# Kernel optimization log

Measured on AMD Instinct MI355X. Metric: run time of the kernel, lower is better.

## Reference

```python
import jax, jax.numpy as jnp
import numpy as np

N_QUBITS = 11
DIM = 2 ** N_QUBITS
N_LAYERS = 6  # the circuit repeats the RY/CZ block 6 times


def _apply_ry(state, wire, theta):
    """Apply RY(theta) on `wire`. state: [N] + [2]*N_QUBITS (real, since RY/CZ are real).
    theta is scalar (shared weight) or [N] (per-sample input angle)."""
    half = theta * 0.5
    c, s = jnp.cos(half), jnp.sin(half)
    if c.ndim == 1:  # per-sample angle -> broadcast over remaining qubit axes
        bshape = (c.shape[0],) + (1,) * (N_QUBITS - 1)
        c = c.reshape(bshape)
        s = s.reshape(bshape)
    st = jnp.moveaxis(state, wire + 1, -1)  # [..., 2]
    s0, s1 = st[..., 0], st[..., 1]
    # RY = [[cos, -sin], [sin, cos]] acting on the qubit amplitude pair
    st = jnp.stack([c * s0 - s * s1, s * s0 + c * s1], axis=-1)
    return jnp.moveaxis(st, -1, wire + 1)


def _apply_cz(state, w1, w2):
    """CZ: flip sign of amplitudes where both qubits are |1>."""
    def bit(w):
        shp = [1] * (N_QUBITS + 1)
        shp[w + 1] = 2
        return jnp.array([0.0, 1.0], state.dtype).reshape(shp)
    sign = 1.0 - 2.0 * bit(w1) * bit(w2)
    return state * sign


def _circuit(angles, weights):
    # angles: [N, N_QUBITS] per-sample RY input angles; weights: [N_QUBITS]
    N = angles.shape[0]
    state = jnp.zeros((N, DIM), angles.dtype).at[:, 0].set(1.0)  # |0...0>
    state = state.reshape((N,) + (2,) * N_QUBITS)
    for i in range(N_QUBITS):
        state = _apply_ry(state, i, angles[:, i])
    for _ in range(N_LAYERS):
        for i in range(N_QUBITS):
            state = _apply_ry(state, i, weights[i])
            state = _apply_cz(state, i, (i + 1) % N_QUBITS)
    probs = state.reshape(N, DIM) ** 2  # real state -> |amp|^2
    # PauliZ expectation per wire; wire 0 is the most-significant bit (PennyLane order)
    bits = (jnp.arange(DIM)[:, None] >> jnp.arange(N_QUBITS - 1, -1, -1)[None, :]) & 1
    z = (1.0 - 2.0 * bits).astype(angles.dtype)  # [DIM, N_QUBITS]
    return probs @ z  # [N, N_QUBITS]


def setup_inputs() -> dict:
    key = jax.random.key(0)
    kx, kw = jax.random.split(key)
    x = jax.random.normal(kx, (8, 256, 16), dtype=jnp.float32)
    weights = jax.random.normal(kw, (N_QUBITS,), dtype=jnp.float32)
    return {"x": x, "weights": weights}


def reference(x, weights):
    B, T, _ = x.shape
    # every (b, t) sample is an independent circuit -> batch them all together
    angles = x[:, :, :N_QUBITS].reshape(B * T, N_QUBITS)
    out = _circuit(angles, weights)  # [B*T, N_QUBITS]
    return out.reshape(B, T, N_QUBITS)
```

## Files before the change

kernel.cpp:

```cpp
#include <hip/hip_runtime.h>

#define NQ 11


typedef float f32x2 __attribute__((ext_vector_type(2)));

__device__ __forceinline__ f32x2 b2(float s) { f32x2 r; r.x = s; r.y = s; return r; }
__device__ __forceinline__ f32x2 fma2(f32x2 a, f32x2 b, f32x2 c) {
    return __builtin_elementwise_fma(a, b, c);
}

template <int CTRL>
__device__ __forceinline__ float dpp_mov(float x) {
    const int xi = __builtin_bit_cast(int, x);
    return __builtin_bit_cast(float,
        __builtin_amdgcn_update_dpp(xi, xi, CTRL, 0xf, 0xf, false));
}
#define DPP_XOR1 0xB1
#define DPP_XOR2 0x4E
#define DPP_XOR3 0x1B
#define DPP_XOR7 0x141
#define DPP_XOR8 0x128

#define RY_K_F(KB, KSB, C, S)                                                \
    _Pragma("unroll")                                                        \
    for (int g = 0; g < 8; ++g) {                                            \
        const int k0 = ((g >> (KB)) << ((KB) + 1)) | (g & ((1 << (KB)) - 1));\
        const int k1 = k0 | (1 << (KB));                                     \
        const f32x2 a_ = v2[k0], b_ = v2[k1];                                \
        const f32x2 Cv = b2(C), Sv = b2(S);                                  \
        if (k0 & (KSB)) {                                   \
            v2[k0] = fma2(Cv, a_, Sv * b_);                                  \
            v2[k1] = fma2(Sv, a_, -(Cv * b_));                               \
        } else {                                                             \
            v2[k0] = fma2(Cv, a_, -(Sv * b_));                               \
            v2[k1] = fma2(Sv, a_, Cv * b_);                                  \
        }                                                                    \
    }

#define RY_LANE2(PGETX, CV, SV)                                              \
    _Pragma("unroll")                                                        \
    for (int k = 0; k < 16; ++k) {                                           \
        f32x2 pa_;                                                           \
        pa_.x = PGETX(v2[k].x);                                              \
        pa_.y = PGETX(v2[k].y);                                              \
        v2[k] = fma2(CV, v2[k], (SV) * pa_);                                 \
    }

__global__ __launch_bounds__(256, 2) void qru_kernel(
    const float* __restrict__ x,
    const float* __restrict__ w,
    float* __restrict__ out)
{
    const int lane = threadIdx.x & 63;
    const int n    = blockIdx.x * 4 + (threadIdx.x >> 6);

    const float4 xa = *(const float4*)(x + n * 16);
    const float4 xb = *(const float4*)(x + n * 16 + 4);
    const float4 xc = *(const float4*)(x + n * 16 + 8);
    const float xv[NQ] = {xa.x, xa.y, xa.z, xa.w, xb.x, xb.y, xb.z, xb.w,
                          xc.x, xc.y, xc.z};
    float ci[NQ], si[NQ];
#pragma unroll
    for (int q = 0; q < NQ; ++q) {
        const float h = xv[q] * 0.5f;
        si[q] = __sinf(h); ci[q] = __cosf(h);
    }
    float cw[NQ], sw[NQ];
#pragma unroll
    for (int q = 0; q < NQ; ++q) {
        const float h = w[q] * 0.5f;
        sw[q] = __sinf(h); cw[q] = __cosf(h);
    }

    const float laneF =
        ((lane & 32) ? si[5]  : ci[5])  *
        ((lane & 16) ? si[6]  : ci[6])  *
        ((lane & 8)  ? si[7]  : ci[7])  *
        ((lane & 4)  ? si[8]  : ci[8])  *
        ((lane & 2)  ? si[9]  : ci[9])  *
        ((lane & 1)  ? si[10] : ci[10]);

    f32x2 v2[16];
#pragma unroll
    for (int k = 0; k < 16; ++k) {
        const float base = laneF * ((k & 8) ? si[0] : ci[0])
                                 * ((k & 4) ? si[1] : ci[1])
                                 * ((k & 2) ? si[2] : ci[2])
                                 * ((k & 1) ? si[3] : ci[3]);
        v2[k].x = base * ci[4];
        v2[k].y = base * si[4];
    }

    const float X0m = (lane & 1) ?  sw[0] : -sw[0];
    const float Y0m = (lane & 1) ? -cw[0] :  cw[0];
    const float SS5 = (lane & 32) ?  sw[5] : -sw[5];
    const float C5m = (lane & 32) ? -cw[5] :  cw[5];
    f32x2 Cv5; Cv5.x = cw[5]; Cv5.y = C5m;
    f32x2 Sv5; Sv5.x = SS5;   Sv5.y = sw[5];
    const f32x2 C6v  = b2(((lane & 48) == 48) ? -cw[6]  : cw[6]);
    const f32x2 S6v  = b2((lane & 48) ? sw[6]  : -sw[6]);
    const f32x2 C7v  = b2(((lane & 24) == 24) ? -cw[7]  : cw[7]);
    const f32x2 S7v  = b2((lane & 24) ? sw[7]  : -sw[7]);
    const f32x2 C8v  = b2(((lane & 12) == 12) ? -cw[8]  : cw[8]);
    const f32x2 S8v  = b2((lane & 12) ? sw[8]  : -sw[8]);
    const f32x2 C9v  = b2(((lane & 6)  == 6)  ? -cw[9]  : cw[9]);
    const f32x2 S9v  = b2((lane & 6)  ? sw[9]  : -sw[9]);
    const f32x2 C10v = b2(((lane & 3)  == 3)  ? -cw[10] : cw[10]);
    const f32x2 S10v = b2((lane & 3)  ? sw[10] : -sw[10]);

    f32x2 C4p; C4p.x = cw[4]; C4p.y =  cw[4];
    f32x2 S4p; S4p.x = -sw[4]; S4p.y = sw[4];
    f32x2 C4m; C4m.x = cw[4]; C4m.y = -cw[4];
    f32x2 S4m; S4m.x = sw[4]; S4m.y =  sw[4];

    auto shfl32 = [](float t) { return __shfl_xor(t, 32); };
    auto shfl16 = [](float t) { return __shfl_xor(t, 16); };
    auto dppx8  = [](float t) { return dpp_mov<DPP_XOR8>(t); };
    auto dppx4  = [](float t) { return dpp_mov<DPP_XOR3>(dpp_mov<DPP_XOR7>(t)); };
    auto dppx2  = [](float t) { return dpp_mov<DPP_XOR2>(t); };
    auto dppx1  = [](float t) { return dpp_mov<DPP_XOR1>(t); };

    auto layer = [&](float X0, float Y0) {
        {
            const f32x2 c0 = b2(cw[0]), s0 = b2(sw[0]);
            const f32x2 x0 = b2(X0),    y0 = b2(Y0);
#pragma unroll
            for (int k = 0; k < 8; ++k) {
                const f32x2 a_ = v2[k], b_ = v2[k | 8];
                v2[k]     = fma2(c0, a_, x0 * b_);
                v2[k | 8] = fma2(s0, a_, y0 * b_);
            }
        }
        RY_K_F(2, 8, cw[1], sw[1])
        RY_K_F(1, 4, cw[2], sw[2])
        RY_K_F(0, 2, cw[3], sw[3])

#pragma unroll
        for (int k = 0; k < 16; ++k) {
            const f32x2 s_ = __builtin_shufflevector(v2[k], v2[k], 1, 0);
            v2[k] = (k & 1) ? fma2(C4m, v2[k], S4m * s_)
                            : fma2(C4p, v2[k], S4p * s_);
        }

        RY_LANE2(shfl32, Cv5, Sv5)
        RY_LANE2(shfl16, C6v, S6v)
        RY_LANE2(dppx8,  C7v, S7v)
        RY_LANE2(dppx4,  C8v, S8v)
        RY_LANE2(dppx2,  C9v, S9v)
        RY_LANE2(dppx1,  C10v, S10v)
    };

    layer(-sw[0], cw[0]);
#pragma unroll 1
    for (int l = 1; l < 6; ++l) layer(X0m, Y0m);

    f32x2 T = b2(0.f), A3 = b2(0.f), A2 = b2(0.f), A1 = b2(0.f), A0 = b2(0.f);
#pragma unroll
    for (int k = 0; k < 16; ++k) {
        const f32x2 p = v2[k] * v2[k];
        T = T + p;
        if (k & 8) A3 = A3 + p;
        if (k & 4) A2 = A2 + p;
        if (k & 2) A1 = A1 + p;
        if (k & 1) A0 = A0 + p;
    }
    const float tot = T.x + T.y;

    float q[NQ];
    q[0] = tot - 2.f * (A3.x + A3.y);
    q[1] = tot - 2.f * (A2.x + A2.y);
    q[2] = tot - 2.f * (A1.x + A1.y);
    q[3] = tot - 2.f * (A0.x + A0.y);
    q[4] = tot - 2.f * T.y;
    q[5]  = (lane & 32) ? -tot : tot;
    q[6]  = (lane & 16) ? -tot : tot;
    q[7]  = (lane & 8)  ? -tot : tot;
    q[8]  = (lane & 4)  ? -tot : tot;
    q[9]  = (lane & 2)  ? -tot : tot;
    q[10] = (lane & 1)  ? -tot : tot;

#pragma unroll
    for (int wq = 0; wq < NQ; ++wq) {
        float a = q[wq];
        a += __shfl_xor(a, 32);
        a += __shfl_xor(a, 16);
        a += dpp_mov<DPP_XOR8>(a);
        a += dpp_mov<DPP_XOR3>(dpp_mov<DPP_XOR7>(a));
        a += dpp_mov<DPP_XOR2>(a);
        a += dpp_mov<DPP_XOR1>(a);
        q[wq] = a;
    }

    if (lane == 0) {
#pragma unroll
        for (int wq = 0; wq < NQ; ++wq) out[n * 11 + wq] = q[wq];
    }
}

extern "C" void kernel_launch(void* const* d_in, const int* in_sizes, int n_in,
                              void* d_out, int out_size, void* d_ws, size_t ws_size,
                              hipStream_t stream) {
    const float* x = (const float*)d_in[0];
    const float* w = (const float*)d_in[1];
    float* out = (float*)d_out;

    qru_kernel<<<512, 256, 0, stream>>>(x, w, out);
}
```

Before: 25.65 us.

## Process two circuits per wavefront to increase ILP and halve grid size

```diff
diff --git a/kernel.cpp b/kernel.cpp
--- a/kernel.cpp
+++ b/kernel.cpp
@@ -22,49 +22,79 @@
 #define DPP_XOR7 0x141
 #define DPP_XOR8 0x128
 
-#define RY_K_F(KB, KSB, C, S)                                                \
-    _Pragma("unroll")                                                        \
-    for (int g = 0; g < 8; ++g) {                                            \
-        const int k0 = ((g >> (KB)) << ((KB) + 1)) | (g & ((1 << (KB)) - 1));\
-        const int k1 = k0 | (1 << (KB));                                     \
-        const f32x2 a_ = v2[k0], b_ = v2[k1];                                \
+#define RY_K_F2(KB, KSB, C, S)                                               \
+    {                                                                        \
         const f32x2 Cv = b2(C), Sv = b2(S);                                  \
-        if (k0 & (KSB)) {                                   \
-            v2[k0] = fma2(Cv, a_, Sv * b_);                                  \
-            v2[k1] = fma2(Sv, a_, -(Cv * b_));                               \
-        } else {                                                             \
-            v2[k0] = fma2(Cv, a_, -(Sv * b_));                               \
-            v2[k1] = fma2(Sv, a_, Cv * b_);                                  \
+        _Pragma("unroll")                                                    \
+        for (int g = 0; g < 8; ++g) {                                        \
+            const int k0 = ((g >> (KB)) << ((KB) + 1)) | (g & ((1 << (KB)) - 1)); \
+            const int k1 = k0 | (1 << (KB));                                 \
+            const f32x2 aA = vA[k0], bA = vA[k1];                            \
+            const f32x2 aB = vB[k0], bB = vB[k1];                            \
+            if (k0 & (KSB)) {                                                \
+                vA[k0] = fma2(Cv, aA, Sv * bA);                              \
+                vA[k1] = fma2(Sv, aA, -(Cv * bA));                           \
+                vB[k0] = fma2(Cv, aB, Sv * bB);                              \
+                vB[k1] = fma2(Sv, aB, -(Cv * bB));                           \
+            } else {                                                         \
+                vA[k0] = fma2(Cv, aA, -(Sv * bA));                           \
+                vA[k1] = fma2(Sv, aA, Cv * bA);                              \
+                vB[k0] = fma2(Cv, aB, -(Sv * bB));                           \
+                vB[k1] = fma2(Sv, aB, Cv * bB);                              \
+            }                                                                \
         }                                                                    \
     }
 
-#define RY_LANE2(PGETX, CV, SV)                                              \
+#define RY_DS2(SHFL, CV, SV)                                                 \
+    {                                                                        \
+        f32x2 pA[16], pB[16];                                                \
+        _Pragma("unroll")                                                    \
+        for (int k = 0; k < 16; ++k) {                                       \
+            pA[k].x = SHFL(vA[k].x); pA[k].y = SHFL(vA[k].y);                \
+            pB[k].x = SHFL(vB[k].x); pB[k].y = SHFL(vB[k].y);                \
+        }                                                                    \
+        _Pragma("unroll")                                                    \
+        for (int k = 0; k < 16; ++k) {                                       \
+            vA[k] = fma2(CV, vA[k], (SV) * pA[k]);                           \
+            vB[k] = fma2(CV, vB[k], (SV) * pB[k]);                           \
+        }                                                                    \
+    }
+
+#define RY_DPP2(PGETX, CV, SV)                                               \
     _Pragma("unroll")                                                        \
     for (int k = 0; k < 16; ++k) {                                           \
-        f32x2 pa_;                                                           \
-        pa_.x = PGETX(v2[k].x);                                              \
-        pa_.y = PGETX(v2[k].y);                                              \
-        v2[k] = fma2(CV, v2[k], (SV) * pa_);                                 \
-    }
-
-__global__ __launch_bounds__(256, 2) void qru_kernel(
+        f32x2 pa, pb;                                                        \
+        pa.x = PGETX(vA[k].x); pa.y = PGETX(vA[k].y);                        \
+        pb.x = PGETX(vB[k].x); pb.y = PGETX(vB[k].y);                        \
+        vA[k] = fma2(CV, vA[k], (SV) * pa);                                  \
+        vB[k] = fma2(CV, vB[k], (SV) * pb);                                  \
+    }
+
+__global__ __launch_bounds__(256, 1) void qru_kernel(
     const float* __restrict__ x,
     const float* __restrict__ w,
     float* __restrict__ out)
 {
     const int lane = threadIdx.x & 63;
-    const int n    = blockIdx.x * 4 + (threadIdx.x >> 6);
-
-    const float4 xa = *(const float4*)(x + n * 16);
-    const float4 xb = *(const float4*)(x + n * 16 + 4);
-    const float4 xc = *(const float4*)(x + n * 16 + 8);
-    const float xv[NQ] = {xa.x, xa.y, xa.z, xa.w, xb.x, xb.y, xb.z, xb.w,
-                          xc.x, xc.y, xc.z};
-    float ci[NQ], si[NQ];
+    const int g    = blockIdx.x * 4 + (threadIdx.x >> 6);
+    const int nA   = 2 * g, nB = 2 * g + 1;
+
+    const float4 a0 = *(const float4*)(x + nA * 16);
+    const float4 a1 = *(const float4*)(x + nA * 16 + 4);
+    const float4 a2 = *(const float4*)(x + nA * 16 + 8);
+    const float4 b0 = *(const float4*)(x + nB * 16);
+    const float4 b1 = *(const float4*)(x + nB * 16 + 4);
+    const float4 b2_ = *(const float4*)(x + nB * 16 + 8);
+    const float xvA[NQ] = {a0.x, a0.y, a0.z, a0.w, a1.x, a1.y, a1.z, a1.w,
+                           a2.x, a2.y, a2.z};
+    const float xvB[NQ] = {b0.x, b0.y, b0.z, b0.w, b1.x, b1.y, b1.z, b1.w,
+                           b2_.x, b2_.y, b2_.z};
+    float ciA[NQ], siA[NQ], ciB[NQ], siB[NQ];
 #pragma unroll
     for (int q = 0; q < NQ; ++q) {
-        const float h = xv[q] * 0.5f;
-        si[q] = __sinf(h); ci[q] = __cosf(h);
+        const float hA = xvA[q] * 0.5f, hB = xvB[q] * 0.5f;
+        siA[q] = __sinf(hA); ciA[q] = __cosf(hA);
+        siB[q] = __sinf(hB); ciB[q] = __cosf(hB);
     }
     float cw[NQ], sw[NQ];
 #pragma unroll
@@ -73,23 +103,36 @@
         sw[q] = __sinf(h); cw[q] = __cosf(h);
     }
 
-    const float laneF =
-        ((lane & 32) ? si[5]  : ci[5])  *
-        ((lane & 16) ? si[6]  : ci[6])  *
-        ((lane & 8)  ? si[7]  : ci[7])  *
-        ((lane & 4)  ? si[8]  : ci[8])  *
-        ((lane & 2)  ? si[9]  : ci[9])  *
-        ((lane & 1)  ? si[10] : ci[10]);
-
-    f32x2 v2[16];
+    const float laneFA =
+        ((lane & 32) ? siA[5]  : ciA[5])  *
+        ((lane & 16) ? siA[6]  : ciA[6])  *
+        ((lane & 8)  ? siA[7]  : ciA[7])  *
+        ((lane & 4)  ? siA[8]  : ciA[8])  *
+        ((lane & 2)  ? siA[9]  : ciA[9])  *
+        ((lane & 1)  ? siA[10] : ciA[10]);
+    const float laneFB =
+        ((lane & 32) ? siB[5]  : ciB[5])  *
+        ((lane & 16) ? siB[6]  : ciB[6])  *
+        ((lane & 8)  ? siB[7]  : ciB[7])  *
+        ((lane & 4)  ? siB[8]  : ciB[8])  *
+        ((lane & 2)  ? siB[9]  : ciB[9])  *
+        ((lane & 1)  ? siB[10] : ciB[10]);
+
+    f32x2 vA[16], vB[16];
 #pragma unroll
     for (int k = 0; k < 16; ++k) {
-        const float base = laneF * ((k & 8) ? si[0] : ci[0])
-                                 * ((k & 4) ? si[1] : ci[1])
-                                 * ((k & 2) ? si[2] : ci[2])
-                                 * ((k & 1) ? si[3] : ci[3]);
-        v2[k].x = base * ci[4];
-        v2[k].y = base * si[4];
+        const float bA = laneFA * ((k & 8) ? siA[0] : ciA[0])
+                                * ((k & 4) ? siA[1] : ciA[1])
+                                * ((k & 2) ? siA[2] : ciA[2])
+                                * ((k & 1) ? siA[3] : ciA[3]);
+        vA[k].x = bA * ciA[4];
+        vA[k].y = bA * siA[4];
+        const float bB = laneFB * ((k & 8) ? siB[0] : ciB[0])
+                                * ((k & 4) ? siB[1] : ciB[1])
+                                * ((k & 2) ? siB[2] : ciB[2])
+                                * ((k & 1) ? siB[3] : ciB[3]);
+        vB[k].x = bB * ciB[4];
+        vB[k].y = bB * siB[4];
     }
 
     const float X0m = (lane & 1) ?  sw[0] : -sw[0];
@@ -109,10 +152,10 @@
     const f32x2 C10v = b2(((lane & 3)  == 3)  ? -cw[10] : cw[10]);
     const f32x2 S10v = b2((lane & 3)  ? sw[10] : -sw[10]);
 
-    f32x2 C4p; C4p.x = cw[4]; C4p.y =  cw[4];
-    f32x2 S4p; S4p.x = -sw[4]; S4p.y = sw[4];
-    f32x2 C4m; C4m.x = cw[4]; C4m.y = -cw[4];
-    f32x2 S4m; S4m.x = sw[4]; S4m.y =  sw[4];
+    f32x2 C4p; C4p.x = cw[4];  C4p.y =  cw[4];
+    f32x2 S4p; S4p.x = -sw[4]; S4p.y =  sw[4];
+    f32x2 C4m; C4m.x = cw[4];  C4m.y = -cw[4];
+    f32x2 S4m; S4m.x = sw[4];  S4m.y =  sw[4];
 
     auto shfl32 = [](float t) { return __shfl_xor(t, 32); };
     auto shfl16 = [](float t) { return __shfl_xor(t, 16); };
@@ -127,74 +170,94 @@
             const f32x2 x0 = b2(X0),    y0 = b2(Y0);
 #pragma unroll
             for (int k = 0; k < 8; ++k) {
-                const f32x2 a_ = v2[k], b_ = v2[k | 8];
-                v2[k]     = fma2(c0, a_, x0 * b_);
-                v2[k | 8] = fma2(s0, a_, y0 * b_);
+                const f32x2 aA = vA[k], bA = vA[k | 8];
+                vA[k]     = fma2(c0, aA, x0 * bA);
+                vA[k | 8] = fma2(s0, aA, y0 * bA);
+                const f32x2 aB = vB[k], bB = vB[k | 8];
+                vB[k]     = fma2(c0, aB, x0 * bB);
+                vB[k | 8] = fma2(s0, aB, y0 * bB);
             }
         }
-        RY_K_F(2, 8, cw[1], sw[1])
-        RY_K_F(1, 4, cw[2], sw[2])
-        RY_K_F(0, 2, cw[3], sw[3])
+        RY_K_F2(2, 8, cw[1], sw[1])
+        RY_K_F2(1, 4, cw[2], sw[2])
+        RY_K_F2(0, 2, cw[3], sw[3])
 
 #pragma unroll
         for (int k = 0; k < 16; ++k) {
-            const f32x2 s_ = __builtin_shufflevector(v2[k], v2[k], 1, 0);
-            v2[k] = (k & 1) ? fma2(C4m, v2[k], S4m * s_)
-                            : fma2(C4p, v2[k], S4p * s_);
+            const f32x2 sA = __builtin_shufflevector(vA[k], vA[k], 1, 0);
+            const f32x2 sB = __builtin_shufflevector(vB[k], vB[k], 1, 0);
+            vA[k] = (k & 1) ? fma2(C4m, vA[k], S4m * sA)
+                            : fma2(C4p, vA[k], S4p * sA);
+            vB[k] = (k & 1) ? fma2(C4m, vB[k], S4m * sB)
+                            : fma2(C4p, vB[k], S4p * sB);
         }
 
-        RY_LANE2(shfl32, Cv5, Sv5)
-        RY_LANE2(shfl16, C6v, S6v)
-        RY_LANE2(dppx8,  C7v, S7v)
-        RY_LANE2(dppx4,  C8v, S8v)
-        RY_LANE2(dppx2,  C9v, S9v)
-        RY_LANE2(dppx1,  C10v, S10v)
+        RY_DS2(shfl32, Cv5, Sv5)
+        RY_DS2(shfl16, C6v, S6v)
+        RY_DPP2(dppx8, C7v,  S7v)
+        RY_DPP2(dppx4, C8v,  S8v)
+        RY_DPP2(dppx2, C9v,  S9v)
+        RY_DPP2(dppx1, C10v, S10v)
     };
 
     layer(-sw[0], cw[0]);
 #pragma unroll 1
     for (int l = 1; l < 6; ++l) layer(X0m, Y0m);
 
-    f32x2 T = b2(0.f), A3 = b2(0.f), A2 = b2(0.f), A1 = b2(0.f), A0 = b2(0.f);
+    f32x2 TA = b2(0.f), A3 = b2(0.f), A2 = b2(0.f), A1 = b2(0.f), A0 = b2(0.f);
+    f32x2 TB = b2(0.f), B3 = b2(0.f), B2 = b2(0.f), B1 = b2(0.f), B0 = b2(0.f);
 #pragma unroll
     for (int k = 0; k < 16; ++k) {
-        const f32x2 p = v2[k] * v2[k];
-        T = T + p;
-        if (k & 8) A3 = A3 + p;
-        if (k & 4) A2 = A2 + p;
-        if (k & 2) A1 = A1 + p;
-        if (k & 1) A0 = A0 + p;
-    }
-    const float tot = T.x + T.y;
-
-    float q[NQ];
-    q[0] = tot - 2.f * (A3.x + A3.y);
-    q[1] = tot - 2.f * (A2.x + A2.y);
-    q[2] = tot - 2.f * (A1.x + A1.y);
-    q[3] = tot - 2.f * (A0.x + A0.y);
-    q[4] = tot - 2.f * T.y;
-    q[5]  = (lane & 32) ? -tot : tot;
-    q[6]  = (lane & 16) ? -tot : tot;
-    q[7]  = (lane & 8)  ? -tot : tot;
-    q[8]  = (lane & 4)  ? -tot : tot;
-    q[9]  = (lane & 2)  ? -tot : tot;
-    q[10] = (lane & 1)  ? -tot : tot;
-
+        const f32x2 pA = vA[k] * vA[k];
+        const f32x2 pB = vB[k] * vB[k];
+        TA = TA + pA;  TB = TB + pB;
+        if (k & 8) { A3 = A3 + pA; B3 = B3 + pB; }
+        if (k & 4) { A2 = A2 + pA; B2 = B2 + pB; }
+        if (k & 2) { A1 = A1 + pA; B1 = B1 + pB; }
+        if (k & 1) { A0 = A0 + pA; B0 = B0 + pB; }
+    }
+    const float totA = TA.x + TA.y, totB = TB.x + TB.y;
+
+    float qA[NQ], qB[NQ];
+    qA[0] = totA - 2.f * (A3.x + A3.y);  qB[0] = totB - 2.f * (B3.x + B3.y);
+    qA[1] = totA - 2.f * (A2.x + A2.y);  qB[1] = totB - 2.f * (B2.x + B2.y);
+    qA[2] = totA - 2.f * (A1.x + A1.y);  qB[2] = totB - 2.f * (B1.x + B1.y);
+    qA[3] = totA - 2.f * (A0.x + A0.y);  qB[3] = totB - 2.f * (B0.x + B0.y);
+    qA[4] = totA - 2.f * TA.y;           qB[4] = totB - 2.f * TB.y;
+    qA[5]  = (lane & 32) ? -totA : totA; qB[5]  = (lane & 32) ? -totB : totB;
+    qA[6]  = (lane & 16) ? -totA : totA; qB[6]  = (lane & 16) ? -totB : totB;
+    qA[7]  = (lane & 8)  ? -totA : totA; qB[7]  = (lane & 8)  ? -totB : totB;
+    qA[8]  = (lane & 4)  ? -totA : totA; qB[8]  = (lane & 4)  ? -totB : totB;
+    qA[9]  = (lane & 2)  ? -totA : totA; qB[9]  = (lane & 2)  ? -totB : totB;
+    qA[10] = (lane & 1)  ? -totA : totA; qB[10] = (lane & 1)  ? -totB : totB;
+
+#pragma unroll
+    for (int wq = 0; wq < NQ; ++wq) { qA[wq] += __shfl_xor(qA[wq], 32);
+                                      qB[wq] += __shfl_xor(qB[wq], 32); }
+#pragma unroll
+    for (int wq = 0; wq < NQ; ++wq) { qA[wq] += __shfl_xor(qA[wq], 16);
+                                      qB[wq] += __shfl_xor(qB[wq], 16); }
+#pragma unroll
+    for (int wq = 0; wq < NQ; ++wq) { qA[wq] += dpp_mov<DPP_XOR8>(qA[wq]);
+                                      qB[wq] += dpp_mov<DPP_XOR8>(qB[wq]); }
 #pragma unroll
     for (int wq = 0; wq < NQ; ++wq) {
-        float a = q[wq];
-        a += __shfl_xor(a, 32);
-        a += __shfl_xor(a, 16);
-        a += dpp_mov<DPP_XOR8>(a);
-        a += dpp_mov<DPP_XOR3>(dpp_mov<DPP_XOR7>(a));
-        a += dpp_mov<DPP_XOR2>(a);
-        a += dpp_mov<DPP_XOR1>(a);
-        q[wq] = a;
-    }
+        qA[wq] += dpp_mov<DPP_XOR3>(dpp_mov<DPP_XOR7>(qA[wq]));
+        qB[wq] += dpp_mov<DPP_XOR3>(dpp_mov<DPP_XOR7>(qB[wq]));
+    }
+#pragma unroll
+    for (int wq = 0; wq < NQ; ++wq) { qA[wq] += dpp_mov<DPP_XOR2>(qA[wq]);
+                                      qB[wq] += dpp_mov<DPP_XOR2>(qB[wq]); }
+#pragma unroll
+    for (int wq = 0; wq < NQ; ++wq) { qA[wq] += dpp_mov<DPP_XOR1>(qA[wq]);
+                                      qB[wq] += dpp_mov<DPP_XOR1>(qB[wq]); }
 
     if (lane == 0) {
 #pragma unroll
-        for (int wq = 0; wq < NQ; ++wq) out[n * 11 + wq] = q[wq];
+        for (int wq = 0; wq < NQ; ++wq) {
+            out[nA * NQ + wq] = qA[wq];
+            out[nB * NQ + wq] = qB[wq];
+        }
     }
 }
 
@@ -205,5 +268,5 @@
     const float* w = (const float*)d_in[1];
     float* out = (float*)d_out;
 
-    qru_kernel<<<512, 256, 0, stream>>>(x, w, out);
-}
+    qru_kernel<<<256, 256, 0, stream>>>(x, w, out);
+}
```

After: 29.87 us. 16.4% more time.
